# Kernel tuning notes

Hardware: AMD Instinct MI355X
Metric: run time of the kernel (lower is better)

The kernel has to match this reference:

```python
import jax, jax.numpy as jnp
import numpy as np

QW, KW = 64, 128          # atom query / key window sizes
PAD = (KW - QW) // 2      # halo on each side of the key window
DEPTH, HEADS = 3, 4

def ln(x):
    m = jnp.mean(x, -1, keepdims=True)
    v = jnp.var(x, -1, keepdims=True)
    return (x - m) * jax.lax.rsqrt(v + 1e-5)

def q_windows(x):
    # x: (B, N, ...) -> (B, n, QW, ...); N assumed multiple of QW
    B, N = x.shape[0], x.shape[1]
    n = N // QW
    return x.reshape((B, n, QW) + x.shape[2:])

def k_windows(x):
    # x: (B, N, ...) -> (B, n, KW, ...) sliding key windows with zero halo padding
    B, N = x.shape[0], x.shape[1]
    n = N // QW
    pad_cfg = [(0, 0), (PAD, n * QW + PAD - N)] + [(0, 0)] * (x.ndim - 2)
    xp = jnp.pad(x, pad_cfg)
    idx = jnp.arange(n)[:, None] * QW + jnp.arange(KW)[None, :]
    return xp[:, idx]


def setup_inputs() -> dict:
    key = jax.random.key(0)
    ks = jax.random.split(key, 24)
    B, N, DS, DP, DT, NT = 2, 8192, 128, 16, 384, 1024
    w = lambda k, shp: (jax.random.normal(k, shp, jnp.float32) / np.sqrt(shp[-2])).astype(jnp.float32)
    inp = {
        'ref_pos': jax.random.normal(ks[0], (B, N, 3), jnp.float32),
        'ref_charge': jax.random.normal(ks[1], (B, N, 1), jnp.float32),
        'ref_mask': jnp.ones((B, N, 1), jnp.float32),
        'ref_element': jax.random.uniform(ks[2], (B, N, 128), jnp.float32),
        'ref_atom_name_chars': jax.random.uniform(ks[3], (B, N, 256), jnp.float32),
        'W_single': w(ks[4], (389, DS)),
        'W_pair': w(ks[5], (5, DP)),
        'W_outer': w(ks[6], (DS, 2 * DP)),
        'Wp_ff1': w(ks[7], (DP, 4 * DP)),
        'Wp_ff2': w(ks[8], (4 * DP, DP)),
        'Wq': w(ks[9], (DEPTH, DS, DS)),
        'Wk': w(ks[10], (DEPTH, DS, DS)),
        'Wv': w(ks[11], (DEPTH, DS, DS)),
        'Wo': w(ks[12], (DEPTH, DS, DS)),
        'Wb': w(ks[13], (DP, HEADS)),
        'Wff1': w(ks[14], (DEPTH, DS, 4 * DS)),
        'Wff2': w(ks[15], (DEPTH, 4 * DS, DS)),
        'W_out': w(ks[16], (DS, DT)),
        'ref_space_uid': jnp.sort(jax.random.randint(ks[17], (B, N), 0, NT), axis=-1),
        'atom_to_token_idx': jnp.sort(jax.random.randint(ks[18], (B, N), 0, NT), axis=-1),
        'n_tokens': NT,
    }
    return inp


def reference(ref_pos, ref_charge, ref_mask, ref_element, ref_atom_name_chars,
              W_single, W_pair, W_outer, Wp_ff1, Wp_ff2,
              Wq, Wk, Wv, Wo, Wb, Wff1, Wff2, W_out,
              ref_space_uid, atom_to_token_idx, n_tokens):
    B, N, _ = ref_pos.shape
    n = N // QW
    feats = jnp.concatenate([ref_pos, ref_charge, ref_mask, ref_element, ref_atom_name_chars], -1)
    s = feats @ W_single                                    # (B,N,DS) atom single repr

    # windowed pairwise geometric features
    pos_i, pos_j = q_windows(ref_pos), k_windows(ref_pos)   # (B,n,QW,3), (B,n,KW,3)
    uid_i, uid_j = q_windows(ref_space_uid), k_windows(ref_space_uid)
    dij = pos_i[:, :, :, None, :] - pos_j[:, :, None, :, :]  # (B,n,QW,KW,3)
    inv = 1.0 / (1.0 + jnp.sum(dij * dij, -1, keepdims=True))
    bij = (uid_i[:, :, :, None] == uid_j[:, :, None, :])
    pf = jnp.concatenate([dij, inv, bij[..., None].astype(dij.dtype)], -1)  # (...,5)
    pair = (pf @ W_pair) * bij[..., None].astype(dij.dtype)  # (B,n,QW,KW,DP)

    # pairwise outer-add from relu(single): Linear(DS->2*DP) split into i/j halves
    p = jax.nn.relu(s) @ W_outer
    DP = pair.shape[-1]
    pi, pj = p[..., :DP], p[..., DP:]
    pair = pair + q_windows(pi)[:, :, :, None, :] + k_windows(pj)[:, :, None, :, :]
    pair = pair + jax.nn.relu(ln(pair) @ Wp_ff1) @ Wp_ff2    # pair FF (residual)
    bias = jnp.einsum('bnqkc,ch->bnhqk', pair, Wb)           # attn pair bias

    # key validity mask for the halo-padded positions
    kidx = jnp.arange(n)[:, None] * QW + jnp.arange(KW)[None, :] - PAD
    kmask = jnp.where((kidx >= 0) & (kidx < N), 0.0, -1e9).astype(s.dtype)  # (n,KW)

    dh = s.shape[-1] // HEADS
    x = s
    for l in range(DEPTH):
        h = ln(x)
        q = q_windows(h @ Wq[l]).reshape(B, n, QW, HEADS, dh)
        k = k_windows(h @ Wk[l]).reshape(B, n, KW, HEADS, dh)
        v = k_windows(h @ Wv[l]).reshape(B, n, KW, HEADS, dh)
        logits = jnp.einsum('bnqhd,bnkhd->bnhqk', q, k) / np.sqrt(dh)
        logits = logits + bias + kmask[None, :, None, None, :]
        a = jax.nn.softmax(logits, -1)
        o = jnp.einsum('bnhqk,bnkhd->bnqhd', a, v).reshape(B, N, -1) @ Wo[l]
        x = x + o
        x = x + jax.nn.relu(ln(x) @ Wff1[l]) @ Wff2[l]

    tok = jax.nn.relu(x @ W_out)                             # (B,N,DT)

    def seg_mean(src, idx_):
        ssum = jax.ops.segment_sum(src, idx_, num_segments=n_tokens)
        cnt = jax.ops.segment_sum(jnp.ones((src.shape[0],), src.dtype), idx_, num_segments=n_tokens)
        return ssum / jnp.clip(cnt, 1.0)[:, None]

    return jax.vmap(seg_mean)(tok, atom_to_token_idx)        # (B, n_tokens, DT)
```

## Files before the change

kernel.cpp:

```cpp
#include <hip/hip_runtime.h>
#include <hip/hip_bf16.h>

#define QW 64
#define KW 128
#define PADW 32
#define DEPTH 3
#define HEADS 4
#define B_ 2
#define N_ 8192
#define DS 128
#define DP 16
#define DT 384
#define NT 1024
#define NWIN (N_ / QW)
#define DH (DS / HEADS)

typedef unsigned short u16;
typedef __attribute__((ext_vector_type(8))) short short8;
typedef __attribute__((ext_vector_type(4))) float f32x4v;
typedef __attribute__((ext_vector_type(4))) unsigned short us4;
typedef __attribute__((ext_vector_type(2))) short s16x2;

__device__ __forceinline__ u16 f2b(float x) {
    union { float f; unsigned u; } v; v.f = x;
    unsigned r = v.u + 0x7fffu + ((v.u >> 16) & 1u);
    return (u16)(r >> 16);
}
__device__ __forceinline__ float b2f(u16 h) {
    union { unsigned u; float f; } v; v.u = ((unsigned)h) << 16; return v.f;
}
__device__ __forceinline__ unsigned f2b2(float a, float b) {
    __hip_bfloat162 h = __float22bfloat162_rn(make_float2(a, b));
    union { __hip_bfloat162 h; unsigned u; } c; c.h = h; return c.u;
}
__device__ __forceinline__ us4 pack4(float a, float b, float c, float d) {
    union { us4 v; unsigned u[2]; } o;
    o.u[0] = f2b2(a, b);
    o.u[1] = f2b2(c, d);
    return o.v;
}
__device__ __forceinline__ us4 pack4_relu(float a, float b, float c, float d) {
    union { us4 v; s16x2 s[2]; unsigned u[2]; } o;
    o.u[0] = f2b2(a, b);
    o.u[1] = f2b2(c, d);
    o.s[0] = __builtin_elementwise_max(o.s[0], (s16x2)0);
    o.s[1] = __builtin_elementwise_max(o.s[1], (s16x2)0);
    return o.v;
}

template <int CTRL>
__device__ __forceinline__ float fdpp(float x) {
    int r = __builtin_amdgcn_update_dpp(0, __builtin_bit_cast(int, x),
                                        CTRL, 0xF, 0xF, true);
    return __builtin_bit_cast(float, r);
}
__device__ __forceinline__ float sum4_dpp(float x) {
    x += fdpp<0xB1>(x);
    x += fdpp<0x4E>(x);
    return x;
}
__device__ __forceinline__ float sum16_dpp(float x) {
    x += fdpp<0xB1>(x);
    x += fdpp<0x4E>(x);
    x += fdpp<0x124>(x);
    x += fdpp<0x128>(x);
    return x;
}
__device__ __forceinline__ float max16_dpp(float x) {
    x = fmaxf(x, fdpp<0xB1>(x));
    x = fmaxf(x, fdpp<0x4E>(x));
    x = fmaxf(x, fdpp<0x124>(x));
    x = fmaxf(x, fdpp<0x128>(x));
    return x;
}

__global__ __launch_bounds__(256) void convw_kernel(
    const float* __restrict__ Wq, const float* __restrict__ Wk,
    const float* __restrict__ Wv, const float* __restrict__ Wo,
    const float* __restrict__ Wff1, const float* __restrict__ Wff2,
    const float* __restrict__ Wout, const float* __restrict__ Wpff1,
    const float* __restrict__ Wpff2, const float* __restrict__ Wb,
    const float* __restrict__ Wsingle, const float* __restrict__ Wouter,
    u16* __restrict__ qkvT, u16* __restrict__ woT, u16* __restrict__ ff1T,
    u16* __restrict__ ff2T, u16* __restrict__ woutT,
    u16* __restrict__ w1T32, u16* __restrict__ wcatT,
    u16* __restrict__ wsT, u16* __restrict__ woutrT)
{
    int idx = blockIdx.x * 256 + threadIdx.x;
    if (idx < 3 * 384 * 128) {
        int l = idx / (384 * 128), r = idx % (384 * 128);
        int n = r / 128, k = r % 128;
        const float* W = (n < 128) ? Wq : (n < 256) ? Wk : Wv;
        qkvT[idx] = f2b(W[(size_t)l * 16384 + k * 128 + (n & 127)]);
    }
    if (idx < 3 * 128 * 128) {
        int l = idx / 16384, r = idx % 16384;
        int n = r / 128, k = r % 128;
        woT[idx] = f2b(Wo[(size_t)l * 16384 + k * 128 + n]);
    }
    if (idx < 3 * 512 * 128) {
        int l = idx / 65536, r = idx % 65536;
        int n = r / 128, k = r % 128;
        ff1T[idx] = f2b(Wff1[(size_t)l * 65536 + k * 512 + n]);
    }
    if (idx < 3 * 128 * 512) {
        int l = idx / 65536, r = idx % 65536;
        int n = r / 512, k = r % 512;
        ff2T[idx] = f2b(Wff2[(size_t)l * 65536 + k * 128 + n]);
    }
    if (idx < 384 * 128) {
        int n = idx / 128, k = idx % 128;
        woutT[idx] = f2b(Wout[(size_t)k * 384 + n]);
    }
    if (idx < 64 * 32) {
        int n = idx >> 5, k = idx & 31;
        w1T32[idx] = (k < 16) ? f2b(Wpff1[k * 64 + n]) : (u16)0;
    }
    if (idx < 16 * 96) {
        int h = idx / 96, k = idx % 96;
        float s = 0.f;
        if (h < 4) {
            if (k < 16) s = Wb[k * 4 + h];
            else if (k < 80) {
                int j = k - 16;
                for (int c = 0; c < 16; ++c) s += Wpff2[j * 16 + c] * Wb[c * 4 + h];
            }
        }
        wcatT[idx] = f2b(s);
    }
    if (idx < 128 * 416) {
        int n = idx / 416, k = idx % 416;
        float v = 0.f;
        if (k < 128)       v = Wsingle[(5 + k) * 128 + n];
        else if (k < 384)  v = Wsingle[(133 + k - 128) * 128 + n];
        else if (k < 387)  v = Wsingle[(k - 384) * 128 + n];
        else if (k == 387) v = Wsingle[3 * 128 + n];
        else if (k == 388) v = Wsingle[4 * 128 + n];
        wsT[idx] = f2b(v);
    }
    if (idx < 32 * 128) {
        int n = idx >> 7, k = idx & 127;
        woutrT[idx] = f2b(Wouter[k * 32 + n]);
    }
}

__global__ __launch_bounds__(256) void embed_gemm(
    const float* __restrict__ pos, const float* __restrict__ charge,
    const float* __restrict__ mask, const float* __restrict__ elem,
    const float* __restrict__ chars, const u16* __restrict__ wsT,
    const u16* __restrict__ woutrT, const u16* __restrict__ qkv0T,
    float* __restrict__ X, float* __restrict__ P, u16* __restrict__ QKVb)
{
    __shared__ __align__(16) u16 As[64 * 424];
    __shared__ float redS[64][4];
    const int LNOFF = 64 * 136;
    int tid = threadIdx.x;
    int row0 = blockIdx.x * 64;

    #pragma unroll
    for (int it = 0; it < 8; ++it) {
        int idx = tid + it * 256;
        int r = idx >> 5, c4 = idx & 31;
        f32x4v v = *(const f32x4v*)(elem + (size_t)(row0 + r) * 128 + c4 * 4);
        *(us4*)&As[r * 424 + c4 * 4] = pack4(v[0], v[1], v[2], v[3]);
    }
    #pragma unroll
    for (int it = 0; it < 16; ++it) {
        int idx = tid + it * 256;
        int r = idx >> 6, c4 = idx & 63;
        f32x4v v = *(const f32x4v*)(chars + (size_t)(row0 + r) * 256 + c4 * 4);
        *(us4*)&As[r * 424 + 128 + c4 * 4] = pack4(v[0], v[1], v[2], v[3]);
    }
    if (tid < 64) {
        int g = row0 + tid;
        As[tid * 424 + 384] = f2b(pos[g * 3]);
        As[tid * 424 + 385] = f2b(pos[g * 3 + 1]);
        As[tid * 424 + 386] = f2b(pos[g * 3 + 2]);
        As[tid * 424 + 387] = f2b(charge[g]);
        As[tid * 424 + 388] = f2b(mask[g]);
        for (int c = 389; c < 416; ++c) As[tid * 424 + c] = 0;
    }
    __syncthreads();

    int wv = tid >> 6, lane = tid & 63, quad = lane >> 4, l16 = lane & 15;
    int wm = (wv & 1) * 32, wn = (wv >> 1) * 64;
    f32x4v acc[2][4];
    #pragma unroll
    for (int i = 0; i < 2; ++i)
        #pragma unroll
        for (int j = 0; j < 4; ++j) acc[i][j] = (f32x4v){0.f, 0.f, 0.f, 0.f};

    #pragma unroll
    for (int kk = 0; kk < 13; ++kk) {
        short8 a0 = *(short8*)&As[(wm + l16) * 424 + kk * 32 + quad * 8];
        short8 a1 = *(short8*)&As[(wm + 16 + l16) * 424 + kk * 32 + quad * 8];
        #pragma unroll
        for (int nt = 0; nt < 4; ++nt) {
            short8 bw = *(const short8*)&wsT[(size_t)(wn + nt * 16 + l16) * 416 +
                                             kk * 32 + quad * 8];
            acc[0][nt] = __builtin_amdgcn_mfma_f32_16x16x32_bf16(a0, bw, acc[0][nt], 0, 0, 0);
            acc[1][nt] = __builtin_amdgcn_mfma_f32_16x16x32_bf16(a1, bw, acc[1][nt], 0, 0, 0);
        }
    }
    __syncthreads();

    #pragma unroll
    for (int mt = 0; mt < 2; ++mt) {
        #pragma unroll
        for (int r = 0; r < 4; ++r) {
            int lrow = wm + mt * 16 + quad * 4 + r;
            int row = row0 + lrow;
            float s = 0.f, ss = 0.f;
            #pragma unroll
            for (int nt = 0; nt < 4; ++nt) {
                float v = acc[mt][nt][r];
                int col = wn + nt * 16 + l16;
                X[(size_t)row * DS + col] = v;
                As[lrow * 136 + col] = f2b(fmaxf(v, 0.f));
                s += v; ss += v * v;
            }
            s  = sum16_dpp(s);
            ss = sum16_dpp(ss);
            if (l16 == 0) {
                redS[lrow][(wv >> 1) * 2]     = s;
                redS[lrow][(wv >> 1) * 2 + 1] = ss;
            }
        }
    }
    __syncthreads();

    #pragma unroll
    for (int mt = 0; mt < 2; ++mt)
        #pragma unroll
        for (int r = 0; r < 4; ++r) {
            int lrow = wm + mt * 16 + quad * 4 + r;
            f32x4v rv = *(f32x4v*)&redS[lrow][0];
            float s = rv[0] + rv[2], ss = rv[1] + rv[3];
            float m = s * (1.f / 128.f);
            float var = ss * (1.f / 128.f) - m * m;
            float rs = __builtin_amdgcn_rsqf(var + 1e-5f);
            #pragma unroll
            for (int nt = 0; nt < 4; ++nt) {
                int col = wn + nt * 16 + l16;
                As[LNOFF + lrow * 136 + col] = f2b((acc[mt][nt][r] - m) * rs);
            }
        }

    {
        f32x4v pacc[2];
        pacc[0] = (f32x4v){0.f, 0.f, 0.f, 0.f};
        pacc[1] = (f32x4v){0.f, 0.f, 0.f, 0.f};
        #pragma unroll
        for (int ks = 0; ks < 4; ++ks) {
            short8 a = *(short8*)&As[(wv * 16 + l16) * 136 + ks * 32 + quad * 8];
            #pragma unroll
            for (int nt = 0; nt < 2; ++nt) {
                short8 bw = *(const short8*)&woutrT[(size_t)(nt * 16 + l16) * 128 +
                                                    ks * 32 + quad * 8];
                pacc[nt] = __builtin_amdgcn_mfma_f32_16x16x32_bf16(a, bw, pacc[nt], 0, 0, 0);
            }
        }
        #pragma unroll
        for (int nt = 0; nt < 2; ++nt)
            #pragma unroll
            for (int r = 0; r < 4; ++r) {
                int row = row0 + wv * 16 + quad * 4 + r;
                P[(size_t)row * 32 + nt * 16 + l16] = pacc[nt][r];
            }
    }
    __syncthreads();

    for (int c = 0; c < 3; ++c) {
        int n0c = c * 128;
        f32x4v qa[2][4];
        #pragma unroll
        for (int i = 0; i < 2; ++i)
            #pragma unroll
            for (int j = 0; j < 4; ++j) qa[i][j] = (f32x4v){0.f, 0.f, 0.f, 0.f};
        #pragma unroll
        for (int ks = 0; ks < 4; ++ks) {
            short8 a0 = *(short8*)&As[LNOFF + (wm + l16) * 136 + ks * 32 + quad * 8];
            short8 a1 = *(short8*)&As[LNOFF + (wm + 16 + l16) * 136 + ks * 32 + quad * 8];
            #pragma unroll
            for (int nt = 0; nt < 4; ++nt) {
                short8 bw = *(const short8*)&qkv0T[(size_t)(n0c + wn + nt * 16 + l16) * 128 +
                                                   ks * 32 + quad * 8];
                qa[0][nt] = __builtin_amdgcn_mfma_f32_16x16x32_bf16(a0, bw, qa[0][nt], 0, 0, 0);
                qa[1][nt] = __builtin_amdgcn_mfma_f32_16x16x32_bf16(a1, bw, qa[1][nt], 0, 0, 0);
            }
        }
        #pragma unroll
        for (int mt = 0; mt < 2; ++mt)
            #pragma unroll
            for (int nt = 0; nt < 4; ++nt)
                #pragma unroll
                for (int r = 0; r < 4; ++r) {
                    int row = row0 + wm + mt * 16 + quad * 4 + r;
                    int col = n0c + wn + nt * 16 + l16;
                    QKVb[(size_t)row * 384 + col] = f2b(qa[mt][nt][r]);
                }
    }
}

__global__ __launch_bounds__(256) void bias_kernel(
    const float* __restrict__ pos, const int* __restrict__ uid,
    const float* __restrict__ P, const float* __restrict__ Wpair,
    const u16* __restrict__ w1T32, const u16* __restrict__ wcatT,
    u16* __restrict__ BIASb)
{
    __shared__ __align__(16) float posjS[128][4];
    __shared__ __align__(16) u16 lpS[4][16 * 24];
    __shared__ __align__(16) u16 A2S[4][16 * 104];

    int tid = threadIdx.x;
    int b  = blockIdx.x >> 11;
    int w  = (blockIdx.x >> 4) & 127;
    int qg = blockIdx.x & 15;

    if (tid < 128) {
        int r = tid;
        int jk = w * QW + r - PADW;
        bool valid = (jk >= 0) && (jk < N_);
        int gk = b * N_ + jk;
        float x = 0.f, y = 0.f, zz = 0.f; int u = 0;
        if (valid) { x = pos[gk * 3]; y = pos[gk * 3 + 1]; zz = pos[gk * 3 + 2]; u = uid[gk]; }
        posjS[r][0] = x; posjS[r][1] = y; posjS[r][2] = zz;
        ((int*)posjS[r])[3] = u;
    }

    int wv = tid >> 6, lane = tid & 63, quad = lane >> 4, l16 = lane & 15;
    int cl = lane >> 2, cg = lane & 3;
    int q = qg * 4 + wv;
    int gq = b * N_ + w * QW + q;

    float xi = pos[gq * 3], yi = pos[gq * 3 + 1], zi = pos[gq * 3 + 2];
    int ui = uid[gq];
    f32x4v pi4 = *(const f32x4v*)(P + (size_t)gq * 32 + cg * 4);
    f32x4v wp[5];
    #pragma unroll
    for (int f = 0; f < 5; ++f)
        wp[f] = *(const f32x4v*)(Wpair + f * 16 + cg * 4);
    short8 w1f[4], wcat[3];
    #pragma unroll
    for (int nt = 0; nt < 4; ++nt)
        w1f[nt] = *(const short8*)&w1T32[(nt * 16 + l16) * 32 + quad * 8];
    #pragma unroll
    for (int ks = 0; ks < 3; ++ks)
        wcat[ks] = *(const short8*)&wcatT[l16 * 96 + ks * 32 + quad * 8];

    f32x4v pjv[8];
    #pragma unroll
    for (int t = 0; t < 8; ++t) {
        int jk = w * QW + t * 16 + cl - PADW;
        bool valid = (jk >= 0) && (jk < N_);
        int gk = b * N_ + jk;
        f32x4v v = (f32x4v){0.f, 0.f, 0.f, 0.f};
        if (valid) v = *(const f32x4v*)(P + (size_t)gk * 32 + 16 + cg * 4);
        pjv[t] = v;
    }

    *(us4*)&A2S[wv][l16 * 104 + 80 + quad * 4] = (us4){0, 0, 0, 0};
    __syncthreads();

    size_t bbase = ((size_t)(b * NWIN + w) * HEADS) * (QW * KW);
    const short8 zero8 = (short8){0, 0, 0, 0, 0, 0, 0, 0};

    #pragma unroll 2
    for (int t = 0; t < 8; ++t) {
        int kk1 = t * 16 + cl;
        f32x4v pj4 = *(const f32x4v*)&posjS[kk1][0];
        float xj = pj4[0], yj = pj4[1], zj = pj4[2];
        int uj = __float_as_int(pj4[3]);
        float dx = xi - xj, dy = yi - yj, dz = zi - zj;
        float inv = __builtin_amdgcn_rcpf(1.f + dx * dx + dy * dy + dz * dz);
        float bf = (ui == uj) ? 1.f : 0.f;
        float pr[4];
        #pragma unroll
        for (int j = 0; j < 4; ++j) {
            float s = fmaf(dx, wp[0][j], fmaf(dy, wp[1][j],
                      fmaf(dz, wp[2][j], fmaf(inv, wp[3][j], wp[4][j]))));
            pr[j] = fmaf(bf, s, pi4[j] + pjv[t][j]);
        }
        float sum = pr[0] + pr[1] + pr[2] + pr[3];
        sum = sum4_dpp(sum);
        float m = sum * (1.f / 16.f);
        float d0 = pr[0] - m, d1 = pr[1] - m, d2 = pr[2] - m, d3 = pr[3] - m;
        float vs = d0 * d0 + d1 * d1 + d2 * d2 + d3 * d3;
        vs = sum4_dpp(vs);
        float rstd = __builtin_amdgcn_rsqf(vs * (1.f / 16.f) + 1e-5f);
        *(us4*)&lpS[wv][cl * 24 + cg * 4] =
            pack4(d0 * rstd, d1 * rstd, d2 * rstd, d3 * rstd);
        *(us4*)&A2S[wv][cl * 104 + cg * 4] = pack4(pr[0], pr[1], pr[2], pr[3]);

        short8 blp = zero8;
        if (quad < 2) blp = *(short8*)&lpS[wv][l16 * 24 + quad * 8];
        #pragma unroll
        for (int nt = 0; nt < 4; ++nt) {
            f32x4v z4 = (f32x4v){0.f, 0.f, 0.f, 0.f};
            z4 = __builtin_amdgcn_mfma_f32_16x16x32_bf16(w1f[nt], blp, z4, 0, 0, 0);
            *(us4*)&A2S[wv][l16 * 104 + 16 + nt * 16 + quad * 4] =
                pack4_relu(z4[0], z4[1], z4[2], z4[3]);
        }
        f32x4v acc = (f32x4v){0.f, 0.f, 0.f, 0.f};
        #pragma unroll
        for (int ks = 0; ks < 3; ++ks) {
            short8 a2 = *(short8*)&A2S[wv][l16 * 104 + ks * 32 + quad * 8];
            acc = __builtin_amdgcn_mfma_f32_16x16x32_bf16(a2, wcat[ks], acc, 0, 0, 0);
        }
        if (l16 < 4) {
            *(us4*)&BIASb[bbase + (size_t)l16 * (QW * KW) + q * KW +
                          t * 16 + quad * 4] = pack4(acc[0], acc[1], acc[2], acc[3]);
        }
    }
}

template <bool LAST>
__global__ __launch_bounds__(256) void wo_ff_fused(
    const u16* __restrict__ Ob, const u16* __restrict__ woT,
    const u16* __restrict__ w1T, const u16* __restrict__ w2T,
    const u16* __restrict__ auxT, float* __restrict__ X,
    u16* __restrict__ OutB)
{
    __shared__ __align__(16) u16 As[32 * 136];
    __shared__ __align__(16) u16 Hs[32 * 520];
    __shared__ float redS[32][4];
    int tid = threadIdx.x;
    int row0 = blockIdx.x * 32;
    int wv = tid >> 6, lane = tid & 63, quad = lane >> 4, l16 = lane & 15;
    int wm = (wv & 1) * 16, wn = (wv >> 1) * 64;

    #pragma unroll
    for (int it = 0; it < 2; ++it) {
        int idx = tid + it * 256;
        int r = idx >> 4, c8 = idx & 15;
        *(short8*)&As[r * 136 + c8 * 8] =
            *(const short8*)&Ob[(size_t)(row0 + r) * 128 + c8 * 8];
    }
    __syncthreads();

    f32x4v acc[4];
    #pragma unroll
    for (int j = 0; j < 4; ++j) acc[j] = (f32x4v){0.f, 0.f, 0.f, 0.f};
    #pragma unroll
    for (int ks = 0; ks < 4; ++ks) {
        short8 a = *(short8*)&As[(wm + l16) * 136 + ks * 32 + quad * 8];
        #pragma unroll
        for (int nt = 0; nt < 4; ++nt) {
            short8 b = *(const short8*)&woT[(size_t)(wn + nt * 16 + l16) * 128 +
                                            ks * 32 + quad * 8];
            acc[nt] = __builtin_amdgcn_mfma_f32_16x16x32_bf16(a, b, acc[nt], 0, 0, 0);
        }
    }
    __syncthreads();

    #pragma unroll
    for (int r = 0; r < 4; ++r) {
        int lrow = wm + quad * 4 + r;
        int row = row0 + lrow;
        float s = 0.f, ss = 0.f;
        #pragma unroll
        for (int nt = 0; nt < 4; ++nt) {
            int col = wn + nt * 16 + l16;
            float v = acc[nt][r] + X[(size_t)row * DS + col];
            acc[nt][r] = v;
            s += v; ss += v * v;
        }
        s  = sum16_dpp(s);
        ss = sum16_dpp(ss);
        if (l16 == 0) {
            redS[lrow][(wv >> 1) * 2]     = s;
            redS[lrow][(wv >> 1) * 2 + 1] = ss;
        }
    }
    __syncthreads();

    #pragma unroll
    for (int r = 0; r < 4; ++r) {
        int lrow = wm + quad * 4 + r;
        f32x4v rv = *(f32x4v*)&redS[lrow][0];
        float s = rv[0] + rv[2], ss = rv[1] + rv[3];
        float m = s * (1.f / 128.f);
        float var = ss * (1.f / 128.f) - m * m;
        float rs = __builtin_amdgcn_rsqf(var + 1e-5f);
        #pragma unroll
        for (int nt = 0; nt < 4; ++nt) {
            int col = wn + nt * 16 + l16;
            As[lrow * 136 + col] = f2b((acc[nt][r] - m) * rs);
        }
    }
    __syncthreads();

    {
        short8 brow[2][4];
        #pragma unroll
        for (int nt = 0; nt < 2; ++nt)
            #pragma unroll
            for (int ks = 0; ks < 4; ++ks)
                brow[nt][ks] = *(short8*)&As[(nt * 16 + l16) * 136 + ks * 32 + quad * 8];
        #pragma unroll
        for (int mt = 0; mt < 8; ++mt) {
            int j0 = wv * 128 + mt * 16;
            f32x4v c0 = (f32x4v){0.f, 0.f, 0.f, 0.f};
            f32x4v c1 = (f32x4v){0.f, 0.f, 0.f, 0.f};
            #pragma unroll
            for (int ks = 0; ks < 4; ++ks) {
                short8 aw = *(const short8*)&w1T[(size_t)(j0 + l16) * 128 +
                                                 ks * 32 + quad * 8];
                c0 = __builtin_amdgcn_mfma_f32_16x16x32_bf16(aw, brow[0][ks], c0, 0, 0, 0);
                c1 = __builtin_amdgcn_mfma_f32_16x16x32_bf16(aw, brow[1][ks], c1, 0, 0, 0);
            }
            *(us4*)&Hs[l16 * 520 + j0 + quad * 4] =
                pack4_relu(c0[0], c0[1], c0[2], c0[3]);
            *(us4*)&Hs[(16 + l16) * 520 + j0 + quad * 4] =
                pack4_relu(c1[0], c1[1], c1[2], c1[3]);
        }
    }
    __syncthreads();

    f32x4v acc2[4];
    #pragma unroll
    for (int j = 0; j < 4; ++j) acc2[j] = (f32x4v){0.f, 0.f, 0.f, 0.f};
    #pragma unroll
    for (int ks = 0; ks < 16; ++ks) {
        short8 a = *(short8*)&Hs[(wm + l16) * 520 + ks * 32 + quad * 8];
        #pragma unroll
        for (int nt = 0; nt < 4; ++nt) {
            short8 b = *(const short8*)&w2T[(size_t)(wn + nt * 16 + l16) * 512 +
                                            ks * 32 + quad * 8];
            acc2[nt] = __builtin_amdgcn_mfma_f32_16x16x32_bf16(a, b, acc2[nt], 0, 0, 0);
        }
    }

    #pragma unroll
    for (int r = 0; r < 4; ++r) {
        int lrow = wm + quad * 4 + r;
        int row = row0 + lrow;
        float s = 0.f, ss = 0.f;
        #pragma unroll
        for (int nt = 0; nt < 4; ++nt) {
            int col = wn + nt * 16 + l16;
            float v = acc2[nt][r] + acc[nt][r];
            acc2[nt][r] = v;
            X[(size_t)row * DS + col] = v;
            s += v; ss += v * v;
        }
        s  = sum16_dpp(s);
        ss = sum16_dpp(ss);
        if (l16 == 0) {
            redS[lrow][(wv >> 1) * 2]     = s;
            redS[lrow][(wv >> 1) * 2 + 1] = ss;
        }
    }
    __syncthreads();

    #pragma unroll
    for (int r = 0; r < 4; ++r) {
        int lrow = wm + quad * 4 + r;
        float m = 0.f, rs = 1.f;
        if (!LAST) {
            f32x4v rv = *(f32x4v*)&redS[lrow][0];
            float s = rv[0] + rv[2], ss = rv[1] + rv[3];
            m = s * (1.f / 128.f);
            float var = ss * (1.f / 128.f) - m * m;
            rs = __builtin_amdgcn_rsqf(var + 1e-5f);
        }
        #pragma unroll
        for (int nt = 0; nt < 4; ++nt) {
            int col = wn + nt * 16 + l16;
            float v = acc2[nt][r];
            As[lrow * 136 + col] = f2b(LAST ? v : (v - m) * rs);
        }
    }
    __syncthreads();

    for (int c = 0; c < 3; ++c) {
        int n0c = c * 128;
        f32x4v qa[4];
        #pragma unroll
        for (int j = 0; j < 4; ++j) qa[j] = (f32x4v){0.f, 0.f, 0.f, 0.f};
        #pragma unroll
        for (int ks = 0; ks < 4; ++ks) {
            short8 a = *(short8*)&As[(wm + l16) * 136 + ks * 32 + quad * 8];
            #pragma unroll
            for (int nt = 0; nt < 4; ++nt) {
                short8 b = *(const short8*)&auxT[(size_t)(n0c + wn + nt * 16 + l16) * 128 +
                                                 ks * 32 + quad * 8];
                qa[nt] = __builtin_amdgcn_mfma_f32_16x16x32_bf16(a, b, qa[nt], 0, 0, 0);
            }
        }
        #pragma unroll
        for (int nt = 0; nt < 4; ++nt)
            #pragma unroll
            for (int r = 0; r < 4; ++r) {
                int row = row0 + wm + quad * 4 + r;
                int col = n0c + wn + nt * 16 + l16;
                float v = qa[nt][r];
                if (LAST) v = fmaxf(v, 0.f);
                OutB[(size_t)row * 384 + col] = f2b(v);
            }
    }
}

__global__ __launch_bounds__(256) void attn_kernel(
    const u16* __restrict__ QKV, const u16* __restrict__ BIASb,
    u16* __restrict__ O)
{
    __shared__ __align__(16) u16 sQ[64 * 40];
    __shared__ __align__(16) u16 sK[128 * 40];
    __shared__ __align__(16) u16 sVt[32 * 152];
    __shared__ __align__(16) u16 sP[64 * 136];

    int tid = threadIdx.x;
    int h = blockIdx.x & 3, w = (blockIdx.x >> 2) & 127, b = blockIdx.x >> 9;
    size_t rowbase = (size_t)b * N_ + w * QW;
    size_t bbase = ((size_t)(b * NWIN + w) * HEADS + h) * (QW * KW);
    const short8 zero8 = (short8){0, 0, 0, 0, 0, 0, 0, 0};
    const bool edge = (w == 0) || (w == NWIN - 1);

    {
        int r = tid >> 2, d8 = (tid & 3) * 8;
        *(short8*)&sQ[r * 40 + d8] =
            *(const short8*)&QKV[(rowbase + r) * 384 + h * DH + d8];
    }
    #pragma unroll
    for (int i = 0; i < 2; ++i) {
        int idx = tid + i * 256;
        int r = idx >> 2, d8 = (idx & 3) * 8;
        int jk = w * QW + r - PADW;
        short8 v = zero8;
        if (jk >= 0 && jk < N_)
            v = *(const short8*)&QKV[((size_t)b * N_ + jk) * 384 + 128 + h * DH + d8];
        *(short8*)&sK[r * 40 + d8] = v;
    }
    {
        int kk = tid >> 1, d0 = (tid & 1) * 16;
        int jk = w * QW + kk - PADW;
        short8 v0 = zero8, v1 = zero8;
        if (jk >= 0 && jk < N_) {
            const u16* src = &QKV[((size_t)b * N_ + jk) * 384 + 256 + h * DH + d0];
            v0 = *(const short8*)src;
            v1 = *(const short8*)(src + 8);
        }
        #pragma unroll
        for (int j = 0; j < 8; ++j) {
            sVt[(d0 + j) * 152 + kk] = (u16)v0[j];
            sVt[(d0 + 8 + j) * 152 + kk] = (u16)v1[j];
        }
    }
    #pragma unroll
    for (int i = 0; i < 4; ++i) {
        int idx = tid + i * 256;
        int q = idx >> 4, c8 = idx & 15;
        *(short8*)&sP[q * 136 + c8 * 8] =
            *(const short8*)&BIASb[bbase + (size_t)q * KW + c8 * 8];
    }
    __syncthreads();

    int wv = tid >> 6, lane = tid & 63, quad = lane >> 4, l16 = lane & 15;
    const float scale = 0.17677669529663687f;

    short8 aq = *(short8*)&sQ[(wv * 16 + l16) * 40 + quad * 8];
    float e[8][4];
    #pragma unroll
    for (int nt = 0; nt < 8; ++nt) {
        short8 bk = *(short8*)&sK[(nt * 16 + l16) * 40 + quad * 8];
        f32x4v acc = (f32x4v){0.f, 0.f, 0.f, 0.f};
        acc = __builtin_amdgcn_mfma_f32_16x16x32_bf16(aq, bk, acc, 0, 0, 0);
        int kk = nt * 16 + l16;
        float msk = 0.f;
        if (edge) {
            int jk = w * QW + kk - PADW;
            msk = (jk >= 0 && jk < N_) ? 0.f : -1e9f;
        }
        #pragma unroll
        for (int r = 0; r < 4; ++r) {
            int q = wv * 16 + quad * 4 + r;
            e[nt][r] = acc[r] * scale + b2f(sP[q * 136 + kk]) + msk;
        }
    }

    #pragma unroll
    for (int r = 0; r < 4; ++r) {
        float m = e[0][r];
        #pragma unroll
        for (int nt = 1; nt < 8; ++nt) m = fmaxf(m, e[nt][r]);
        m = max16_dpp(m);
        float s = 0.f;
        #pragma unroll
        for (int nt = 0; nt < 8; ++nt) {
            float ev = __expf(e[nt][r] - m);
            e[nt][r] = ev;
            s += ev;
        }
        s = sum16_dpp(s);
        float inv = __builtin_amdgcn_rcpf(s);
        #pragma unroll
        for (int nt = 0; nt < 8; ++nt) e[nt][r] *= inv;
    }

    #pragma unroll
    for (int nt = 0; nt < 8; ++nt) {
        int kk = nt * 16 + l16;
        #pragma unroll
        for (int r = 0; r < 4; ++r) {
            int q = wv * 16 + quad * 4 + r;
            sP[q * 136 + kk] = f2b(e[nt][r]);
        }
    }

    short8 ap[4];
    #pragma unroll
    for (int ks = 0; ks < 4; ++ks)
        ap[ks] = *(short8*)&sP[(wv * 16 + l16) * 136 + ks * 32 + quad * 8];
    #pragma unroll
    for (int nt = 0; nt < 2; ++nt) {
        f32x4v acc = (f32x4v){0.f, 0.f, 0.f, 0.f};
        #pragma unroll
        for (int ks = 0; ks < 4; ++ks) {
            short8 bv = *(short8*)&sVt[(nt * 16 + l16) * 152 + ks * 32 + quad * 8];
            acc = __builtin_amdgcn_mfma_f32_16x16x32_bf16(ap[ks], bv, acc, 0, 0, 0);
        }
        int d = nt * 16 + l16;
        #pragma unroll
        for (int r = 0; r < 4; ++r) {
            int q = wv * 16 + quad * 4 + r;
            O[(rowbase + q) * DS + h * DH + d] = f2b(acc[r]);
        }
    }
}

__global__ __launch_bounds__(128) void seg_kernel(
    const u16* __restrict__ TOKb, const int* __restrict__ idx,
    float* __restrict__ out)
{
    int t = blockIdx.x & (NT - 1);
    int b = blockIdx.x >> 10;
    const int* id = idx + (size_t)b * N_;

    int lo = 0, hi = N_;
    while (lo < hi) { int mid = (lo + hi) >> 1; if (id[mid] < t) lo = mid + 1; else hi = mid; }
    int start = lo;
    hi = N_;
    while (lo < hi) { int mid = (lo + hi) >> 1; if (id[mid] < t + 1) lo = mid + 1; else hi = mid; }
    int end = lo;

    float inv = 1.f / fmaxf((float)(end - start), 1.f);
    if (threadIdx.x < 96) {
        int c4 = threadIdx.x * 4;
        f32x4v s = (f32x4v){0.f, 0.f, 0.f, 0.f};
        for (int r = start; r < end; ++r) {
            us4 v = *(const us4*)&TOKb[((size_t)b * N_ + r) * DT + c4];
            s[0] += b2f(v[0]); s[1] += b2f(v[1]);
            s[2] += b2f(v[2]); s[3] += b2f(v[3]);
        }
        s[0] *= inv; s[1] *= inv; s[2] *= inv; s[3] *= inv;
        *(f32x4v*)&out[((size_t)b * NT + t) * DT + c4] = s;
    }
}

extern "C" void kernel_launch(void* const* d_in, const int* in_sizes, int n_in,
                              void* d_out, int out_size, void* d_ws, size_t ws_size,
                              hipStream_t stream)
{
    const float* ref_pos    = (const float*)d_in[0];
    const float* ref_charge = (const float*)d_in[1];
    const float* ref_mask   = (const float*)d_in[2];
    const float* ref_elem   = (const float*)d_in[3];
    const float* ref_chars  = (const float*)d_in[4];
    const float* W_single   = (const float*)d_in[5];
    const float* W_pair     = (const float*)d_in[6];
    const float* W_outer    = (const float*)d_in[7];
    const float* Wp_ff1     = (const float*)d_in[8];
    const float* Wp_ff2     = (const float*)d_in[9];
    const float* Wq         = (const float*)d_in[10];
    const float* Wk         = (const float*)d_in[11];
    const float* Wv         = (const float*)d_in[12];
    const float* Wo         = (const float*)d_in[13];
    const float* Wb         = (const float*)d_in[14];
    const float* Wff1       = (const float*)d_in[15];
    const float* Wff2       = (const float*)d_in[16];
    const float* W_out      = (const float*)d_in[17];
    const int*   uid        = (const int*)d_in[18];
    const int*   a2t        = (const int*)d_in[19];
    float* out = (float*)d_out;

    const size_t ROWS = (size_t)B_ * N_;
    float* ws = (float*)d_ws;
    float* X    = ws;
    float* P    = X + ROWS * DS;
    u16* QKVb   = (u16*)(P + ROWS * 32);
    u16* Ob     = QKVb + ROWS * 384;
    u16* FFb    = Ob + ROWS * DS;
    u16* BIASb  = FFb + ROWS * 512;
    u16* TOKb   = BIASb + (size_t)B_ * NWIN * HEADS * QW * KW;
    u16* LNb    = TOKb + ROWS * DT;
    u16* qkvT   = LNb + ROWS * DS;
    u16* woT    = qkvT + 3 * 384 * 128;
    u16* ff1T   = woT + 3 * 128 * 128;
    u16* ff2T   = ff1T + 3 * 512 * 128;
    u16* woutT  = ff2T + 3 * 128 * 512;
    u16* w1T32  = woutT + 384 * 128;
    u16* wcatT  = w1T32 + 64 * 32;
    u16* wsT    = wcatT + 16 * 96;
    u16* woutrT = wsT + 128 * 416;

    convw_kernel<<<768, 256, 0, stream>>>(Wq, Wk, Wv, Wo, Wff1, Wff2, W_out,
                                          Wp_ff1, Wp_ff2, Wb, W_single, W_outer,
                                          qkvT, woT, ff1T, ff2T, woutT,
                                          w1T32, wcatT, wsT, woutrT);
    embed_gemm<<<ROWS / 64, 256, 0, stream>>>(ref_pos, ref_charge, ref_mask,
                                              ref_elem, ref_chars, wsT, woutrT,
                                              qkvT, X, P, QKVb);
    bias_kernel<<<4096, 256, 0, stream>>>(ref_pos, uid, P, W_pair,
                                          w1T32, wcatT, BIASb);

    for (int l = 0; l < DEPTH; ++l) {
        attn_kernel<<<B_ * NWIN * HEADS, 256, 0, stream>>>(QKVb, BIASb, Ob);
        if (l < DEPTH - 1) {
            wo_ff_fused<false><<<ROWS / 32, 256, 0, stream>>>(
                Ob, woT + (size_t)l * 128 * 128,
                ff1T + (size_t)l * 512 * 128, ff2T + (size_t)l * 128 * 512,
                qkvT + (size_t)(l + 1) * 384 * 128, X, QKVb);
        } else {
            wo_ff_fused<true><<<ROWS / 32, 256, 0, stream>>>(
                Ob, woT + (size_t)l * 128 * 128,
                ff1T + (size_t)l * 512 * 128, ff2T + (size_t)l * 128 * 512,
                woutT, X, TOKb);
        }
    }

    seg_kernel<<<B_ * NT, 128, 0, stream>>>(TOKb, a2t, out);
}
```

Measured before the change: 353.1 us.

## Halve fused Wo/FF row tile to 16 rows and load Q fragments directly

```diff
diff --git a/kernel.cpp b/kernel.cpp
--- a/kernel.cpp
+++ b/kernel.cpp
@@ -421,31 +421,29 @@
     const u16* __restrict__ auxT, float* __restrict__ X,
     u16* __restrict__ OutB)
 {
-    __shared__ __align__(16) u16 As[32 * 136];
-    __shared__ __align__(16) u16 Hs[32 * 520];
-    __shared__ float redS[32][4];
+    __shared__ __align__(16) u16 As[16 * 136];
+    __shared__ __align__(16) u16 Hs[16 * 520];
+    __shared__ __align__(16) float redS[16][8];
     int tid = threadIdx.x;
-    int row0 = blockIdx.x * 32;
+    int row0 = blockIdx.x * 16;
     int wv = tid >> 6, lane = tid & 63, quad = lane >> 4, l16 = lane & 15;
-    int wm = (wv & 1) * 16, wn = (wv >> 1) * 64;
-
-    #pragma unroll
-    for (int it = 0; it < 2; ++it) {
-        int idx = tid + it * 256;
-        int r = idx >> 4, c8 = idx & 15;
+    int wn = wv * 32;
+
+    {
+        int r = tid >> 4, c8 = tid & 15;
         *(short8*)&As[r * 136 + c8 * 8] =
             *(const short8*)&Ob[(size_t)(row0 + r) * 128 + c8 * 8];
     }
     __syncthreads();
 
-    f32x4v acc[4];
-    #pragma unroll
-    for (int j = 0; j < 4; ++j) acc[j] = (f32x4v){0.f, 0.f, 0.f, 0.f};
+    f32x4v acc[2];
+    acc[0] = (f32x4v){0.f, 0.f, 0.f, 0.f};
+    acc[1] = (f32x4v){0.f, 0.f, 0.f, 0.f};
     #pragma unroll
     for (int ks = 0; ks < 4; ++ks) {
-        short8 a = *(short8*)&As[(wm + l16) * 136 + ks * 32 + quad * 8];
-        #pragma unroll
-        for (int nt = 0; nt < 4; ++nt) {
+        short8 a = *(short8*)&As[l16 * 136 + ks * 32 + quad * 8];
+        #pragma unroll
+        for (int nt = 0; nt < 2; ++nt) {
             short8 b = *(const short8*)&woT[(size_t)(wn + nt * 16 + l16) * 128 +
                                             ks * 32 + quad * 8];
             acc[nt] = __builtin_amdgcn_mfma_f32_16x16x32_bf16(a, b, acc[nt], 0, 0, 0);
@@ -455,11 +453,11 @@
 
     #pragma unroll
     for (int r = 0; r < 4; ++r) {
-        int lrow = wm + quad * 4 + r;
+        int lrow = quad * 4 + r;
         int row = row0 + lrow;
         float s = 0.f, ss = 0.f;
         #pragma unroll
-        for (int nt = 0; nt < 4; ++nt) {
+        for (int nt = 0; nt < 2; ++nt) {
             int col = wn + nt * 16 + l16;
             float v = acc[nt][r] + X[(size_t)row * DS + col];
             acc[nt][r] = v;
@@ -468,22 +466,24 @@
         s  = sum16_dpp(s);
         ss = sum16_dpp(ss);
         if (l16 == 0) {
-            redS[lrow][(wv >> 1) * 2]     = s;
-            redS[lrow][(wv >> 1) * 2 + 1] = ss;
+            redS[lrow][wv * 2]     = s;
+            redS[lrow][wv * 2 + 1] = ss;
         }
     }
     __syncthreads();
 
     #pragma unroll
     for (int r = 0; r < 4; ++r) {
-        int lrow = wm + quad * 4 + r;
-        f32x4v rv = *(f32x4v*)&redS[lrow][0];
-        float s = rv[0] + rv[2], ss = rv[1] + rv[3];
+        int lrow = quad * 4 + r;
+        f32x4v rv0 = *(f32x4v*)&redS[lrow][0];
+        f32x4v rv1 = *(f32x4v*)&redS[lrow][4];
+        float s  = rv0[0] + rv0[2] + rv1[0] + rv1[2];
+        float ss = rv0[1] + rv0[3] + rv1[1] + rv1[3];
         float m = s * (1.f / 128.f);
         float var = ss * (1.f / 128.f) - m * m;
         float rs = __builtin_amdgcn_rsqf(var + 1e-5f);
         #pragma unroll
-        for (int nt = 0; nt < 4; ++nt) {
+        for (int nt = 0; nt < 2; ++nt) {
             int col = wn + nt * 16 + l16;
             As[lrow * 136 + col] = f2b((acc[nt][r] - m) * rs);
         }
@@ -491,40 +491,34 @@
     __syncthreads();
 
     {
-        short8 brow[2][4];
-        #pragma unroll
-        for (int nt = 0; nt < 2; ++nt)
-            #pragma unroll
-            for (int ks = 0; ks < 4; ++ks)
-                brow[nt][ks] = *(short8*)&As[(nt * 16 + l16) * 136 + ks * 32 + quad * 8];
+        short8 brow[4];
+        #pragma unroll
+        for (int ks = 0; ks < 4; ++ks)
+            brow[ks] = *(short8*)&As[l16 * 136 + ks * 32 + quad * 8];
         #pragma unroll
         for (int mt = 0; mt < 8; ++mt) {
             int j0 = wv * 128 + mt * 16;
             f32x4v c0 = (f32x4v){0.f, 0.f, 0.f, 0.f};
-            f32x4v c1 = (f32x4v){0.f, 0.f, 0.f, 0.f};
             #pragma unroll
             for (int ks = 0; ks < 4; ++ks) {
                 short8 aw = *(const short8*)&w1T[(size_t)(j0 + l16) * 128 +
                                                  ks * 32 + quad * 8];
-                c0 = __builtin_amdgcn_mfma_f32_16x16x32_bf16(aw, brow[0][ks], c0, 0, 0, 0);
-                c1 = __builtin_amdgcn_mfma_f32_16x16x32_bf16(aw, brow[1][ks], c1, 0, 0, 0);
+                c0 = __builtin_amdgcn_mfma_f32_16x16x32_bf16(aw, brow[ks], c0, 0, 0, 0);
             }
             *(us4*)&Hs[l16 * 520 + j0 + quad * 4] =
                 pack4_relu(c0[0], c0[1], c0[2], c0[3]);
-            *(us4*)&Hs[(16 + l16) * 520 + j0 + quad * 4] =
-                pack4_relu(c1[0], c1[1], c1[2], c1[3]);
-        }
-    }
-    __syncthreads();
-
-    f32x4v acc2[4];
-    #pragma unroll
-    for (int j = 0; j < 4; ++j) acc2[j] = (f32x4v){0.f, 0.f, 0.f, 0.f};
+        }
+    }
+    __syncthreads();
+
+    f32x4v acc2[2];
+    acc2[0] = (f32x4v){0.f, 0.f, 0.f, 0.f};
+    acc2[1] = (f32x4v){0.f, 0.f, 0.f, 0.f};
     #pragma unroll
     for (int ks = 0; ks < 16; ++ks) {
-        short8 a = *(short8*)&Hs[(wm + l16) * 520 + ks * 32 + quad * 8];
-        #pragma unroll
-        for (int nt = 0; nt < 4; ++nt) {
+        short8 a = *(short8*)&Hs[l16 * 520 + ks * 32 + quad * 8];
+        #pragma unroll
+        for (int nt = 0; nt < 2; ++nt) {
             short8 b = *(const short8*)&w2T[(size_t)(wn + nt * 16 + l16) * 512 +
                                             ks * 32 + quad * 8];
             acc2[nt] = __builtin_amdgcn_mfma_f32_16x16x32_bf16(a, b, acc2[nt], 0, 0, 0);
@@ -533,11 +527,11 @@
 
     #pragma unroll
     for (int r = 0; r < 4; ++r) {
-        int lrow = wm + quad * 4 + r;
+        int lrow = quad * 4 + r;
         int row = row0 + lrow;
         float s = 0.f, ss = 0.f;
         #pragma unroll
-        for (int nt = 0; nt < 4; ++nt) {
+        for (int nt = 0; nt < 2; ++nt) {
             int col = wn + nt * 16 + l16;
             float v = acc2[nt][r] + acc[nt][r];
             acc2[nt][r] = v;
@@ -547,25 +541,27 @@
         s  = sum16_dpp(s);
         ss = sum16_dpp(ss);
         if (l16 == 0) {
-            redS[lrow][(wv >> 1) * 2]     = s;
-            redS[lrow][(wv >> 1) * 2 + 1] = ss;
+            redS[lrow][wv * 2]     = s;
+            redS[lrow][wv * 2 + 1] = ss;
         }
     }
     __syncthreads();
 
     #pragma unroll
     for (int r = 0; r < 4; ++r) {
-        int lrow = wm + quad * 4 + r;
+        int lrow = quad * 4 + r;
         float m = 0.f, rs = 1.f;
         if (!LAST) {
-            f32x4v rv = *(f32x4v*)&redS[lrow][0];
-            float s = rv[0] + rv[2], ss = rv[1] + rv[3];
+            f32x4v rv0 = *(f32x4v*)&redS[lrow][0];
+            f32x4v rv1 = *(f32x4v*)&redS[lrow][4];
+            float s  = rv0[0] + rv0[2] + rv1[0] + rv1[2];
+            float ss = rv0[1] + rv0[3] + rv1[1] + rv1[3];
             m = s * (1.f / 128.f);
             float var = ss * (1.f / 128.f) - m * m;
             rs = __builtin_amdgcn_rsqf(var + 1e-5f);
         }
         #pragma unroll
-        for (int nt = 0; nt < 4; ++nt) {
+        for (int nt = 0; nt < 2; ++nt) {
             int col = wn + nt * 16 + l16;
             float v = acc2[nt][r];
             As[lrow * 136 + col] = f2b(LAST ? v : (v - m) * rs);
@@ -573,31 +569,36 @@
     }
     __syncthreads();
 
-    for (int c = 0; c < 3; ++c) {
-        int n0c = c * 128;
-        f32x4v qa[4];
-        #pragma unroll
-        for (int j = 0; j < 4; ++j) qa[j] = (f32x4v){0.f, 0.f, 0.f, 0.f};
-        #pragma unroll
-        for (int ks = 0; ks < 4; ++ks) {
-            short8 a = *(short8*)&As[(wm + l16) * 136 + ks * 32 + quad * 8];
-            #pragma unroll
-            for (int nt = 0; nt < 4; ++nt) {
-                short8 b = *(const short8*)&auxT[(size_t)(n0c + wn + nt * 16 + l16) * 128 +
-                                                 ks * 32 + quad * 8];
-                qa[nt] = __builtin_amdgcn_mfma_f32_16x16x32_bf16(a, b, qa[nt], 0, 0, 0);
+    {
+        short8 arow[4];
+        #pragma unroll
+        for (int ks = 0; ks < 4; ++ks)
+            arow[ks] = *(short8*)&As[l16 * 136 + ks * 32 + quad * 8];
+        for (int c = 0; c < 3; ++c) {
+            int n0c = c * 128;
+            f32x4v qa[2];
+            qa[0] = (f32x4v){0.f, 0.f, 0.f, 0.f};
+            qa[1] = (f32x4v){0.f, 0.f, 0.f, 0.f};
+            #pragma unroll
+            for (int ks = 0; ks < 4; ++ks) {
+                #pragma unroll
+                for (int nt = 0; nt < 2; ++nt) {
+                    short8 b = *(const short8*)&auxT[(size_t)(n0c + wn + nt * 16 + l16) * 128 +
+                                                     ks * 32 + quad * 8];
+                    qa[nt] = __builtin_amdgcn_mfma_f32_16x16x32_bf16(arow[ks], b, qa[nt], 0, 0, 0);
+                }
             }
-        }
-        #pragma unroll
-        for (int nt = 0; nt < 4; ++nt)
-            #pragma unroll
-            for (int r = 0; r < 4; ++r) {
-                int row = row0 + wm + quad * 4 + r;
-                int col = n0c + wn + nt * 16 + l16;
-                float v = qa[nt][r];
-                if (LAST) v = fmaxf(v, 0.f);
-                OutB[(size_t)row * 384 + col] = f2b(v);
-            }
+            #pragma unroll
+            for (int nt = 0; nt < 2; ++nt)
+                #pragma unroll
+                for (int r = 0; r < 4; ++r) {
+                    int row = row0 + quad * 4 + r;
+                    int col = n0c + wn + nt * 16 + l16;
+                    float v = qa[nt][r];
+                    if (LAST) v = fmaxf(v, 0.f);
+                    OutB[(size_t)row * 384 + col] = f2b(v);
+                }
+        }
     }
 }
 
@@ -605,7 +606,6 @@
     const u16* __restrict__ QKV, const u16* __restrict__ BIASb,
     u16* __restrict__ O)
 {
-    __shared__ __align__(16) u16 sQ[64 * 40];
     __shared__ __align__(16) u16 sK[128 * 40];
     __shared__ __align__(16) u16 sVt[32 * 152];
     __shared__ __align__(16) u16 sP[64 * 136];
@@ -617,11 +617,10 @@
     const short8 zero8 = (short8){0, 0, 0, 0, 0, 0, 0, 0};
     const bool edge = (w == 0) || (w == NWIN - 1);
 
-    {
-        int r = tid >> 2, d8 = (tid & 3) * 8;
-        *(short8*)&sQ[r * 40 + d8] =
-            *(const short8*)&QKV[(rowbase + r) * 384 + h * DH + d8];
-    }
+    int wv = tid >> 6, lane = tid & 63, quad = lane >> 4, l16 = lane & 15;
+
+    short8 aq = *(const short8*)&QKV[(rowbase + wv * 16 + l16) * 384 + h * DH + quad * 8];
+
     #pragma unroll
     for (int i = 0; i < 2; ++i) {
         int idx = tid + i * 256;
@@ -656,10 +655,8 @@
     }
     __syncthreads();
 
-    int wv = tid >> 6, lane = tid & 63, quad = lane >> 4, l16 = lane & 15;
     const float scale = 0.17677669529663687f;
 
-    short8 aq = *(short8*)&sQ[(wv * 16 + l16) * 40 + quad * 8];
     float e[8][4];
     #pragma unroll
     for (int nt = 0; nt < 8; ++nt) {
@@ -817,12 +814,12 @@
     for (int l = 0; l < DEPTH; ++l) {
         attn_kernel<<<B_ * NWIN * HEADS, 256, 0, stream>>>(QKVb, BIASb, Ob);
         if (l < DEPTH - 1) {
-            wo_ff_fused<false><<<ROWS / 32, 256, 0, stream>>>(
+            wo_ff_fused<false><<<ROWS / 16, 256, 0, stream>>>(
                 Ob, woT + (size_t)l * 128 * 128,
                 ff1T + (size_t)l * 512 * 128, ff2T + (size_t)l * 128 * 512,
                 qkvT + (size_t)(l + 1) * 384 * 128, X, QKVb);
         } else {
-            wo_ff_fused<true><<<ROWS / 32, 256, 0, stream>>>(
+            wo_ff_fused<true><<<ROWS / 16, 256, 0, stream>>>(
                 Ob, woT + (size_t)l * 128 * 128,
                 ff1T + (size_t)l * 512 * 128, ff2T + (size_t)l * 128 * 512,
                 woutT, X, TOKb);
```

After: 369.0 us. 1.05x slower.
